# Kernel optimization log

Measured on AMD Instinct MI355X. Metric: run time of the kernel, lower is better.

## Reference

```python
import jax, jax.numpy as jnp
import numpy as np

B, S, E = 2, 2048, 1024
H = 16
HD = E // H  # 64


def setup_inputs() -> dict:
    key = jax.random.key(0)
    ks = jax.random.split(key, 9)
    sc = 1.0 / np.sqrt(E)
    return {
        "X": jax.random.normal(ks[0], (B, S, E), jnp.float32),
        "Wq": jax.random.normal(ks[1], (E, E), jnp.float32) * sc,
        "bq": jax.random.normal(ks[2], (E,), jnp.float32) * sc,
        "Wk": jax.random.normal(ks[3], (E, E), jnp.float32) * sc,
        "bk": jax.random.normal(ks[4], (E,), jnp.float32) * sc,
        "Wv": jax.random.normal(ks[5], (E, E), jnp.float32) * sc,
        "bv": jax.random.normal(ks[6], (E,), jnp.float32) * sc,
        "Wo": jax.random.normal(ks[7], (E, E), jnp.float32) * sc,
        "bo": jax.random.normal(ks[8], (E,), jnp.float32) * sc,
    }


def reference(X, Wq, bq, Wk, bk, Wv, bv, Wo, bo):
    b, s, e = X.shape
    # torch Linear: x @ W.T + b (weights stored (out, in))
    Q = X @ Wq.T + bq
    K = X @ Wk.T + bk
    V = X @ Wv.T + bv
    # (b, s, E) -> (b, H, s, HD)
    Q = Q.reshape(b, s, H, HD).transpose(0, 2, 1, 3)
    K = K.reshape(b, s, H, HD).transpose(0, 2, 1, 3)
    V = V.reshape(b, s, H, HD).transpose(0, 2, 1, 3)
    scores = jnp.einsum("bhqd,bhkd->bhqk", Q, K) / np.sqrt(HD).astype(np.float32)
    attn = jax.nn.softmax(scores, axis=-1)
    ctx = jnp.einsum("bhqk,bhkd->bhqd", attn, V)  # (b, H, s, HD)
    # Faithful to original: reshape (b,H,s,HD) -> (b,s,E) WITHOUT permuting heads back
    ctx = ctx.reshape(b, s, e)
    return ctx @ Wo.T + bo
```

## Files before the change

### kernel.cpp

```cpp
#include <hip/hip_runtime.h>


typedef __bf16 bf16x8 __attribute__((ext_vector_type(8)));
typedef __bf16 bf16x4 __attribute__((ext_vector_type(4)));
typedef float f32x4 __attribute__((ext_vector_type(4)));
typedef unsigned short ushort_t;

#define S_LEN 2048
#define E_DIM 1024
#define H_NUM 16
#define HD_DIM 64

__device__ __forceinline__ ushort_t f2bf(float f) {
  union { float f; unsigned u; } v; v.f = f;
  unsigned u = v.u;
  unsigned r = (u + 0x7FFFu + ((u >> 16) & 1u)) >> 16;
  return (ushort_t)r;
}

#define GLDS16(gp, lp)                                              \
  __builtin_amdgcn_global_load_lds(                                 \
      (const __attribute__((address_space(1))) unsigned int*)(gp),  \
      (__attribute__((address_space(3))) unsigned int*)(lp), 16, 0, 0)

__global__ __launch_bounds__(256) void cvt_all(
    const float* __restrict__ X, const float* __restrict__ Wq,
    const float* __restrict__ Wk, const float* __restrict__ Wv,
    const float* __restrict__ Wo, ushort_t* __restrict__ Xbf,
    ushort_t* __restrict__ Wqkv, ushort_t* __restrict__ Wob) {
  int i = blockIdx.x * 256 + threadIdx.x;
  const float* src;
  ushort_t* dst;
  int off;
  if (i < 1048576) {
    src = X; dst = Xbf; off = i;
  } else if (i < 1310720) {
    src = Wq; dst = Wqkv; off = i - 1048576;
  } else if (i < 1572864) {
    src = Wk; dst = Wqkv + (1 << 20); off = i - 1310720;
  } else if (i < 1835008) {
    src = Wv; dst = Wqkv + (2 << 20); off = i - 1572864;
  } else {
    src = Wo; dst = Wob; off = i - 1835008;
  }
  float4 v = ((const float4*)src)[off];
  ushort4 o;
  o.x = f2bf(v.x); o.y = f2bf(v.y); o.z = f2bf(v.z); o.w = f2bf(v.w);
  ((ushort4*)dst)[off] = o;
}

__global__ __launch_bounds__(256) void gemm_qkv(
    const ushort_t* __restrict__ Xbf, const ushort_t* __restrict__ Wqkv,
    const float* __restrict__ bq, const float* __restrict__ bk,
    const float* __restrict__ bv,
    ushort_t* __restrict__ Qb, ushort_t* __restrict__ Kb,
    ushort_t* __restrict__ Vt) {
  __shared__ ushort_t As[128 * 64];
  __shared__ ushort_t Bs[128 * 64];
  const int t = threadIdx.x;
  const int w = t >> 6, lane = t & 63, quad = lane >> 4, lr = lane & 15;
  const int m0 = blockIdx.y * 128, n0 = blockIdx.x * 128;
  const int wm = (w & 1) * 64, wn = (w >> 1) * 64;
  const int matid = n0 >> 10;
  const int nl0 = n0 & 1023;

  const int srow = t >> 3;
  const int gsrc = (t & 7) ^ (srow & 7);
  const ushort_t* Ag = Xbf + (size_t)(m0 + srow) * E_DIM + gsrc * 8;
  const ushort_t* Bg = Wqkv + (size_t)matid * E_DIM * E_DIM +
                       (size_t)(nl0 + srow) * E_DIM + gsrc * 8;

  f32x4 acc[4][4] = {};

  for (int kt = 0; kt < E_DIM / 64; ++kt) {
#pragma unroll
    for (int r = 0; r < 4; r++) {
      GLDS16(Ag + (size_t)r * 32 * E_DIM, As + r * 2048 + t * 8);
      GLDS16(Bg + (size_t)r * 32 * E_DIM, Bs + r * 2048 + t * 8);
    }
    Ag += 64; Bg += 64;
    __syncthreads();
#pragma unroll
    for (int kk = 0; kk < 2; kk++) {
      bf16x8 af[4], bfr[4];
      const int gs0 = (kk * 4 + quad) ^ (lr & 7);
#pragma unroll
      for (int i = 0; i < 4; i++) {
        af[i]  = *(const bf16x8*)(As + (wm + i * 16 + lr) * 64 + gs0 * 8);
        bfr[i] = *(const bf16x8*)(Bs + (wn + i * 16 + lr) * 64 + gs0 * 8);
      }
#pragma unroll
      for (int i = 0; i < 4; i++)
#pragma unroll
        for (int j = 0; j < 4; j++)
          acc[i][j] = __builtin_amdgcn_mfma_f32_16x16x32_bf16(
              af[i], bfr[j], acc[i][j], 0, 0, 0);
    }
    __syncthreads();
  }

  const float* bias_p = (matid == 0) ? bq : (matid == 1) ? bk : bv;
  if (matid < 2) {
    ushort_t* dst = (matid == 0) ? Qb : Kb;
    const float scl = (matid == 0) ? 0.125f : 1.0f;
#pragma unroll
    for (int j = 0; j < 4; j++) {
      int cl = (n0 + wn + j * 16 + lr) & 1023;
      int h = cl >> 6, d = cl & 63;
      float bias = bias_p[cl];
#pragma unroll
      for (int i = 0; i < 4; i++) {
#pragma unroll
        for (int r = 0; r < 4; r++) {
          int row = m0 + wm + i * 16 + quad * 4 + r;
          int bb = row >> 11, ss = row & 2047;
          size_t o = ((size_t)((bb * H_NUM + h) * S_LEN + ss)) * HD_DIM + d;
          dst[o] = f2bf((acc[i][j][r] + bias) * scl);
        }
      }
    }
  } else {
#pragma unroll
    for (int j = 0; j < 4; j++) {
      int cl = (n0 + wn + j * 16 + lr) & 1023;
      int h = cl >> 6, d = cl & 63;
      float bias = bias_p[cl];
#pragma unroll
      for (int i = 0; i < 4; i++) {
#pragma unroll
        for (int r = 0; r < 4; r++) {
          int row = m0 + wm + i * 16 + quad * 4 + r;
          int bb = row >> 11, ss = row & 2047;
          size_t o = ((size_t)((bb * H_NUM + h) * HD_DIM + d)) * S_LEN +
                     (ss & ~63) + ((ss & 15) * 4) + ((ss >> 4) & 3);
          Vt[o] = f2bf(acc[i][j][r] + bias);
        }
      }
    }
  }
}

__global__ __launch_bounds__(256) void attn(
    const ushort_t* __restrict__ Qb, const ushort_t* __restrict__ Kb,
    const ushort_t* __restrict__ Vt, ushort_t* __restrict__ Ctx) {
  __shared__ ushort_t KV[2 * 8192];
  __shared__ ushort_t Ps[64 * 72];
  const int t = threadIdx.x, w = t >> 6, lane = t & 63;
  const int quad = lane >> 4, lr = lane & 15;
  const int bh = blockIdx.y, q0 = blockIdx.x * 64;
  const ushort_t* Qg = Qb + ((size_t)bh * S_LEN + q0) * HD_DIM;
  const ushort_t* Kg = Kb + (size_t)bh * S_LEN * HD_DIM;
  const ushort_t* Vg = Vt + (size_t)bh * HD_DIM * S_LEN;

  const int srow = t >> 3;
  const int gsrc = (t & 7) ^ (srow & 7);

#pragma unroll
  for (int r = 0; r < 2; r++) {
    GLDS16(Qg + (size_t)(r * 32 + srow) * HD_DIM + gsrc * 8,
           Ps + r * 2048 + t * 8);
    GLDS16(Kg + (size_t)(r * 32 + srow) * HD_DIM + gsrc * 8,
           KV + r * 2048 + t * 8);
    GLDS16(Vg + (size_t)(r * 32 + srow) * S_LEN + gsrc * 8,
           KV + 4096 + r * 2048 + t * 8);
  }
  __syncthreads();
  bf16x8 qf[2];
#pragma unroll
  for (int kc = 0; kc < 2; kc++) {
    int gs = (kc * 4 + quad) ^ (lr & 7);
    qf[kc] = *(const bf16x8*)(Ps + (w * 16 + lr) * 64 + gs * 8);
  }
  __syncthreads();

  const ushort_t* kp = Kg + srow * HD_DIM + gsrc * 8 + 64 * HD_DIM;
  const ushort_t* vp = Vg + srow * S_LEN + gsrc * 8 + 64;

  f32x4 cacc[4] = {};
  float psum[4] = {};

  for (int kt = 0; kt < S_LEN / 64; ++kt) {
    const ushort_t* Kbuf = KV + (kt & 1) * 8192;
    const ushort_t* Vbuf = Kbuf + 4096;
    if (kt + 1 < S_LEN / 64) {
      ushort_t* nb = KV + ((kt + 1) & 1) * 8192;
      GLDS16(kp, nb + t * 8);
      GLDS16(kp + 32 * HD_DIM, nb + 2048 + t * 8);
      GLDS16(vp, nb + 4096 + t * 8);
      GLDS16(vp + 32 * S_LEN, nb + 6144 + t * 8);
      kp += 64 * HD_DIM;
      vp += 64;
    }

    f32x4 sacc[4] = {};
#pragma unroll
    for (int nt = 0; nt < 4; nt++) {
#pragma unroll
      for (int kc = 0; kc < 2; kc++) {
        int gs = (kc * 4 + quad) ^ (lr & 7);
        bf16x8 kf = *(const bf16x8*)(Kbuf + (nt * 16 + lr) * 64 + gs * 8);
        sacc[nt] = __builtin_amdgcn_mfma_f32_16x16x32_bf16(
            qf[kc], kf, sacc[nt], 0, 0, 0);
      }
    }

#pragma unroll
    for (int i = 0; i < 4; i++) {
      float p0 = __expf(sacc[0][i]);
      float p1 = __expf(sacc[1][i]);
      float p2 = __expf(sacc[2][i]);
      float p3 = __expf(sacc[3][i]);
      psum[i] += (p0 + p1) + (p2 + p3);
      bf16x4 pv;
      pv[0] = (__bf16)p0; pv[1] = (__bf16)p1;
      pv[2] = (__bf16)p2; pv[3] = (__bf16)p3;
      int row = w * 16 + quad * 4 + i;
      *(bf16x4*)(Ps + row * 72 + lr * 4) = pv;
    }

#pragma unroll
    for (int kc = 0; kc < 2; kc++) {
      bf16x8 pf =
          *(const bf16x8*)(Ps + (w * 16 + lr) * 72 + kc * 32 + quad * 8);
#pragma unroll
      for (int dt = 0; dt < 4; dt++) {
        int gs = (kc * 4 + quad) ^ (lr & 7);
        bf16x8 vf = *(const bf16x8*)(Vbuf + (dt * 16 + lr) * 64 + gs * 8);
        cacc[dt] = __builtin_amdgcn_mfma_f32_16x16x32_bf16(
            pf, vf, cacc[dt], 0, 0, 0);
      }
    }
    __syncthreads();
  }

#pragma unroll
  for (int i = 0; i < 4; i++) {
    float rs = psum[i];
    rs += __shfl_xor(rs, 1);
    rs += __shfl_xor(rs, 2);
    rs += __shfl_xor(rs, 4);
    rs += __shfl_xor(rs, 8);
    float inv = 1.0f / rs;
    int srow2 = q0 + w * 16 + quad * 4 + i;
#pragma unroll
    for (int dt = 0; dt < 4; dt++)
      Ctx[((size_t)bh * S_LEN + srow2) * HD_DIM + dt * 16 + lr] =
          f2bf(cacc[dt][i] * inv);
  }
}

__global__ __launch_bounds__(256) void gemm_out(
    const ushort_t* __restrict__ Cb, const ushort_t* __restrict__ Wob,
    const float* __restrict__ bo, float* __restrict__ out) {
  __shared__ ushort_t As[64 * 64];
  __shared__ ushort_t Bs[64 * 64];
  const int t = threadIdx.x;
  const int w = t >> 6, lane = t & 63, quad = lane >> 4, lr = lane & 15;
  const int m0 = blockIdx.y * 64, n0 = blockIdx.x * 64;
  const int wm = (w & 1) * 32, wn = (w >> 1) * 32;

  const int srow = t >> 3;
  const int gsrc = (t & 7) ^ (srow & 7);
  const ushort_t* Ag = Cb + (size_t)(m0 + srow) * E_DIM + gsrc * 8;
  const ushort_t* Bg = Wob + (size_t)(n0 + srow) * E_DIM + gsrc * 8;

  f32x4 acc[2][2] = {};

  for (int kt = 0; kt < E_DIM / 64; ++kt) {
#pragma unroll
    for (int r = 0; r < 2; r++) {
      GLDS16(Ag + (size_t)r * 32 * E_DIM, As + r * 2048 + t * 8);
      GLDS16(Bg + (size_t)r * 32 * E_DIM, Bs + r * 2048 + t * 8);
    }
    Ag += 64; Bg += 64;
    __syncthreads();
#pragma unroll
    for (int kk = 0; kk < 2; kk++) {
      bf16x8 af[2], bfr[2];
      const int gs0 = (kk * 4 + quad) ^ (lr & 7);
#pragma unroll
      for (int i = 0; i < 2; i++) {
        af[i]  = *(const bf16x8*)(As + (wm + i * 16 + lr) * 64 + gs0 * 8);
        bfr[i] = *(const bf16x8*)(Bs + (wn + i * 16 + lr) * 64 + gs0 * 8);
      }
#pragma unroll
      for (int i = 0; i < 2; i++)
#pragma unroll
        for (int j = 0; j < 2; j++)
          acc[i][j] = __builtin_amdgcn_mfma_f32_16x16x32_bf16(
              af[i], bfr[j], acc[i][j], 0, 0, 0);
    }
    __syncthreads();
  }

#pragma unroll
  for (int j = 0; j < 2; j++) {
    int col = n0 + wn + j * 16 + lr;
    float bias = bo[col];
#pragma unroll
    for (int i = 0; i < 2; i++) {
#pragma unroll
      for (int r = 0; r < 4; r++) {
        int row = m0 + wm + i * 16 + quad * 4 + r;
        out[(size_t)row * E_DIM + col] = acc[i][j][r] + bias;
      }
    }
  }
}

extern "C" void kernel_launch(void* const* d_in, const int* in_sizes, int n_in,
                              void* d_out, int out_size, void* d_ws,
                              size_t ws_size, hipStream_t stream) {
  const float* X  = (const float*)d_in[0];
  const float* bq = (const float*)d_in[2];
  const float* bk = (const float*)d_in[4];
  const float* bv = (const float*)d_in[6];
  const float* Wo = (const float*)d_in[7];
  const float* bo = (const float*)d_in[8];
  float* out = (float*)d_out;

  char* ws = (char*)d_ws;
  ushort_t* Xbf  = (ushort_t*)(ws);
  ushort_t* Wqkv = (ushort_t*)(ws + ((size_t)8 << 20));
  ushort_t* Wob  = (ushort_t*)(ws + ((size_t)14 << 20));
  ushort_t* Qb   = (ushort_t*)(ws + ((size_t)16 << 20));
  ushort_t* Kb   = (ushort_t*)(ws + ((size_t)24 << 20));
  ushort_t* Vt   = (ushort_t*)(ws + ((size_t)32 << 20));
  ushort_t* Cb   = (ushort_t*)(ws + ((size_t)40 << 20));

  cvt_all<<<8192, 256, 0, stream>>>(X, (const float*)d_in[1],
                                    (const float*)d_in[3],
                                    (const float*)d_in[5], Wo, Xbf, Wqkv, Wob);

  gemm_qkv<<<dim3(24, 32), 256, 0, stream>>>(Xbf, Wqkv, bq, bk, bv, Qb, Kb, Vt);
  attn<<<dim3(32, 32), 256, 0, stream>>>(Qb, Kb, Vt, Cb);
  gemm_out<<<dim3(16, 64), 256, 0, stream>>>(Cb, Wob, bo, out);
}
```

Measured before the change: 213.7 us.

## Split K/V buffers with staggered reloads and compute row sums via MFMA

Replaces the double-buffered combined K/V LDS tile with single K and V buffers. The next K tile is loaded right after the QK^T MFMAs finish and the next V tile right after PV, which halves attention LDS use (raising possible occupancy) while still overlapping loads with compute. The softmax row-sum is now an MFMA of P against a vector of ones, replacing per-element adds and the final shuffle reduction. The sum is taken over bf16-rounded P, which matches the numerator. It adds an extra barrier per iteration and a wasted wrap-around load on the last iteration.

```diff
diff --git a/kernel.cpp b/kernel.cpp
--- a/kernel.cpp
+++ b/kernel.cpp
@@ -143,7 +143,8 @@
 __global__ __launch_bounds__(256) void attn(
     const ushort_t* __restrict__ Qb, const ushort_t* __restrict__ Kb,
     const ushort_t* __restrict__ Vt, ushort_t* __restrict__ Ctx) {
-  __shared__ ushort_t KV[2 * 8192];
+  __shared__ ushort_t Ks[64 * 64];
+  __shared__ ushort_t Vs[64 * 64];
   __shared__ ushort_t Ps[64 * 72];
   const int t = threadIdx.x, w = t >> 6, lane = t & 63;
   const int quad = lane >> 4, lr = lane & 15;
@@ -160,9 +161,9 @@
     GLDS16(Qg + (size_t)(r * 32 + srow) * HD_DIM + gsrc * 8,
            Ps + r * 2048 + t * 8);
     GLDS16(Kg + (size_t)(r * 32 + srow) * HD_DIM + gsrc * 8,
-           KV + r * 2048 + t * 8);
+           Ks + r * 2048 + t * 8);
     GLDS16(Vg + (size_t)(r * 32 + srow) * S_LEN + gsrc * 8,
-           KV + 4096 + r * 2048 + t * 8);
+           Vs + r * 2048 + t * 8);
   }
   __syncthreads();
   bf16x8 qf[2];
@@ -171,37 +172,34 @@
     int gs = (kc * 4 + quad) ^ (lr & 7);
     qf[kc] = *(const bf16x8*)(Ps + (w * 16 + lr) * 64 + gs * 8);
   }
-  __syncthreads();
-
-  const ushort_t* kp = Kg + srow * HD_DIM + gsrc * 8 + 64 * HD_DIM;
-  const ushort_t* vp = Vg + srow * S_LEN + gsrc * 8 + 64;
+
+  bf16x8 ones;
+#pragma unroll
+  for (int e = 0; e < 8; e++) ones[e] = (__bf16)1.0f;
 
   f32x4 cacc[4] = {};
-  float psum[4] = {};
+  f32x4 lsum = {};
 
   for (int kt = 0; kt < S_LEN / 64; ++kt) {
-    const ushort_t* Kbuf = KV + (kt & 1) * 8192;
-    const ushort_t* Vbuf = Kbuf + 4096;
-    if (kt + 1 < S_LEN / 64) {
-      ushort_t* nb = KV + ((kt + 1) & 1) * 8192;
-      GLDS16(kp, nb + t * 8);
-      GLDS16(kp + 32 * HD_DIM, nb + 2048 + t * 8);
-      GLDS16(vp, nb + 4096 + t * 8);
-      GLDS16(vp + 32 * S_LEN, nb + 6144 + t * 8);
-      kp += 64 * HD_DIM;
-      vp += 64;
-    }
-
     f32x4 sacc[4] = {};
 #pragma unroll
     for (int nt = 0; nt < 4; nt++) {
 #pragma unroll
       for (int kc = 0; kc < 2; kc++) {
         int gs = (kc * 4 + quad) ^ (lr & 7);
-        bf16x8 kf = *(const bf16x8*)(Kbuf + (nt * 16 + lr) * 64 + gs * 8);
+        bf16x8 kf = *(const bf16x8*)(Ks + (nt * 16 + lr) * 64 + gs * 8);
         sacc[nt] = __builtin_amdgcn_mfma_f32_16x16x32_bf16(
             qf[kc], kf, sacc[nt], 0, 0, 0);
       }
+    }
+    __syncthreads();
+
+    {
+      const int kn = (kt + 1) & (S_LEN / 64 - 1);
+#pragma unroll
+      for (int r = 0; r < 2; r++)
+        GLDS16(Kg + (size_t)(kn * 64 + r * 32 + srow) * HD_DIM + gsrc * 8,
+               Ks + r * 2048 + t * 8);
     }
 
 #pragma unroll
@@ -210,7 +208,6 @@
       float p1 = __expf(sacc[1][i]);
       float p2 = __expf(sacc[2][i]);
       float p3 = __expf(sacc[3][i]);
-      psum[i] += (p0 + p1) + (p2 + p3);
       bf16x4 pv;
       pv[0] = (__bf16)p0; pv[1] = (__bf16)p1;
       pv[2] = (__bf16)p2; pv[3] = (__bf16)p3;
@@ -222,25 +219,29 @@
     for (int kc = 0; kc < 2; kc++) {
       bf16x8 pf =
           *(const bf16x8*)(Ps + (w * 16 + lr) * 72 + kc * 32 + quad * 8);
+      lsum = __builtin_amdgcn_mfma_f32_16x16x32_bf16(pf, ones, lsum, 0, 0, 0);
 #pragma unroll
       for (int dt = 0; dt < 4; dt++) {
         int gs = (kc * 4 + quad) ^ (lr & 7);
-        bf16x8 vf = *(const bf16x8*)(Vbuf + (dt * 16 + lr) * 64 + gs * 8);
+        bf16x8 vf = *(const bf16x8*)(Vs + (dt * 16 + lr) * 64 + gs * 8);
         cacc[dt] = __builtin_amdgcn_mfma_f32_16x16x32_bf16(
             pf, vf, cacc[dt], 0, 0, 0);
       }
     }
     __syncthreads();
+
+    {
+      const int kn = (kt + 1) & (S_LEN / 64 - 1);
+#pragma unroll
+      for (int r = 0; r < 2; r++)
+        GLDS16(Vg + (size_t)(r * 32 + srow) * S_LEN + kn * 64 + gsrc * 8,
+               Vs + r * 2048 + t * 8);
+    }
   }
 
 #pragma unroll
   for (int i = 0; i < 4; i++) {
-    float rs = psum[i];
-    rs += __shfl_xor(rs, 1);
-    rs += __shfl_xor(rs, 2);
-    rs += __shfl_xor(rs, 4);
-    rs += __shfl_xor(rs, 8);
-    float inv = 1.0f / rs;
+    float inv = 1.0f / lsum[i];
     int srow2 = q0 + w * 16 + quad * 4 + i;
 #pragma unroll
     for (int dt = 0; dt < 4; dt++)
```

Result: faster. 196.2 us (-8.2%).
